# Performance work log

Measured on AMD Instinct MI355X. Metric: run time of the kernel, lower is better.

Reference implementation:

```python
import jax, jax.numpy as jnp
import numpy as np

V, E, H, T, S = 100000, 256, 512, 48, 2048
HD = H // 2  # per-direction hidden size


def _lstm_dir(x, h0, c0, Wih, Whh, b, reverse):
    # Single-direction LSTM over (S, E) input; PyTorch gate order i,f,g,o.
    def step(carry, xt):
        h, c = carry
        z = xt @ Wih.T + h @ Whh.T + b  # (4*HD,)
        i, f, g, o = jnp.split(z, 4)
        i = jax.nn.sigmoid(i)
        f = jax.nn.sigmoid(f)
        g = jnp.tanh(g)
        o = jax.nn.sigmoid(o)
        c = f * c + i * g
        h = o * jnp.tanh(c)
        return (h, c), h
    _, hs = jax.lax.scan(step, (h0, c0), x, reverse=reverse)
    return hs  # (S, HD)


def setup_inputs() -> dict:
    key = jax.random.key(0)
    ks = jax.random.split(key, 12)
    scale = 1.0 / np.sqrt(HD)
    inp = {
        "sent": jax.random.randint(ks[0], (S,), 0, V),
        "embed_table": jax.random.normal(ks[1], (V, E), jnp.float32),
        "Wih_f": jax.random.normal(ks[2], (4 * HD, E), jnp.float32) * scale,
        "Whh_f": jax.random.normal(ks[3], (4 * HD, HD), jnp.float32) * scale,
        "b_f": jax.random.normal(ks[4], (4 * HD,), jnp.float32) * scale,
        "Wih_b": jax.random.normal(ks[5], (4 * HD, E), jnp.float32) * scale,
        "Whh_b": jax.random.normal(ks[6], (4 * HD, HD), jnp.float32) * scale,
        "b_b": jax.random.normal(ks[7], (4 * HD,), jnp.float32) * scale,
        "W_out": jax.random.normal(ks[8], (T, H), jnp.float32) * (1.0 / np.sqrt(H)),
        "b_out": jnp.zeros((T,), jnp.float32),
        "transitions": jax.random.normal(ks[9], (T, T), jnp.float32) * 0.01,
        "h0": jax.random.normal(ks[10], (2, HD), jnp.float32),
        "c0": jax.random.normal(ks[11], (2, HD), jnp.float32),
    }
    return inp


def reference(sent, embed_table, Wih_f, Whh_f, b_f, Wih_b, Whh_b, b_b,
              W_out, b_out, transitions, h0, c0):
    x = embed_table[sent]  # (S, E)
    hf = _lstm_dir(x, h0[0], c0[0], Wih_f, Whh_f, b_f, False)
    hb = _lstm_dir(x, h0[1], c0[1], Wih_b, Whh_b, b_b, True)
    lstm_out = jnp.concatenate([hf, hb], axis=-1)  # (S, H)
    feats = lstm_out @ W_out.T + b_out  # (S, T) emission scores

    # Viterbi forward pass: scores[i,j] = prev[i] + trans[i,j] + obs[j]
    def vstep(prev, obs):
        scores = prev[:, None] + transitions + obs[None, :]
        return jnp.max(scores, axis=0), jnp.argmax(scores, axis=0)
    prev, bps = jax.lax.scan(vstep, feats[0], feats[1:])  # bps: (S-1, T)

    last = jnp.argmax(prev)

    # Backtrack: reverse scan collects the tag at each timestep in order.
    def back(cur, bp):
        p = bp[cur]
        return p, p
    _, prevs = jax.lax.scan(back, last, bps, reverse=True)  # (S-1,)
    path = jnp.concatenate([prevs, last[None]])  # (S,)
    return path
```

## Files before the change

kernel.cpp:

```cpp
#include <hip/hip_runtime.h>
#include <hip/hip_bf16.h>
#include <math.h>

#define S   2048
#define E   256
#define HD  256
#define NCOL 2048
#define NT  48
#define NWG 16

#define XZ_OFF      ((size_t)0)
#define XZ_BYTES    ((size_t)S * 2048 * 4)
#define LSTM_OFF    (XZ_OFF + XZ_BYTES)
#define LSTM_BYTES  ((size_t)S * 512 * 4)
#define FEATS_OFF   (LSTM_OFF + LSTM_BYTES)
#define FEATS_BYTES ((size_t)S * NT * 4)
#define HCUR2_OFF   (FEATS_OFF + FEATS_BYTES)
#define HCUR2_BYTES ((size_t)2 * 2 * 256 * 8)
#define BPS_OFF     (HCUR2_OFF + HCUR2_BYTES)
#define BPS_BYTES   ((size_t)S * NT)
#define PATHA_OFF   (BPS_OFF + BPS_BYTES)
#define PATHA_BYTES ((size_t)3072 * 32)

__device__ __forceinline__ void st_pair_dev(uint2* p, uint2 v) {
    asm volatile("global_store_dwordx2 %0, %1, off sc0 sc1"
                 :: "v"(p), "v"(v) : "memory");
}

__device__ __forceinline__ bool try_h16(const uint2* p, unsigned want,
                                        float h16[16]) {
    uint4 a, b, c, d, e, f, g, h;
    asm volatile(
        "global_load_dwordx4 %0, %8, off sc0 sc1\n\t"
        "global_load_dwordx4 %1, %8, off offset:16 sc0 sc1\n\t"
        "global_load_dwordx4 %2, %8, off offset:32 sc0 sc1\n\t"
        "global_load_dwordx4 %3, %8, off offset:48 sc0 sc1\n\t"
        "global_load_dwordx4 %4, %8, off offset:64 sc0 sc1\n\t"
        "global_load_dwordx4 %5, %8, off offset:80 sc0 sc1\n\t"
        "global_load_dwordx4 %6, %8, off offset:96 sc0 sc1\n\t"
        "global_load_dwordx4 %7, %8, off offset:112 sc0 sc1\n\t"
        "s_waitcnt vmcnt(0)"
        : "=&v"(a), "=&v"(b), "=&v"(c), "=&v"(d),
          "=&v"(e), "=&v"(f), "=&v"(g), "=&v"(h)
        : "v"(p)
        : "memory");
    const unsigned bad =
        (a.y ^ want) | (a.w ^ want) | (b.y ^ want) | (b.w ^ want) |
        (c.y ^ want) | (c.w ^ want) | (d.y ^ want) | (d.w ^ want) |
        (e.y ^ want) | (e.w ^ want) | (f.y ^ want) | (f.w ^ want) |
        (g.y ^ want) | (g.w ^ want) | (h.y ^ want) | (h.w ^ want);
    if (bad) return false;
    h16[0]  = __uint_as_float(a.x); h16[1]  = __uint_as_float(a.z);
    h16[2]  = __uint_as_float(b.x); h16[3]  = __uint_as_float(b.z);
    h16[4]  = __uint_as_float(c.x); h16[5]  = __uint_as_float(c.z);
    h16[6]  = __uint_as_float(d.x); h16[7]  = __uint_as_float(d.z);
    h16[8]  = __uint_as_float(e.x); h16[9]  = __uint_as_float(e.z);
    h16[10] = __uint_as_float(f.x); h16[11] = __uint_as_float(f.z);
    h16[12] = __uint_as_float(g.x); h16[13] = __uint_as_float(g.z);
    h16[14] = __uint_as_float(h.x); h16[15] = __uint_as_float(h.z);
    return true;
}

__global__ __launch_bounds__(256) void gemm_xz(
    const int* __restrict__ sent, const float* __restrict__ emb,
    const float* __restrict__ Wih_f, const float* __restrict__ Wih_b,
    const float* __restrict__ b_f, const float* __restrict__ b_b,
    float* __restrict__ xz)
{
    __shared__ float As[16][132];
    __shared__ float Bs[16][132];
    const int tid = threadIdx.x;
    const int bm = blockIdx.x * 128;
    const int bn = blockIdx.y * 128;
    const int tx = tid & 15, ty = tid >> 4;
    const int lm = tid >> 1, kq = (tid & 1) * 8;

    const int srow = sent[bm + lm];
    const float* arow = emb + (size_t)srow * E;
    const int bcol = bn + lm;
    const float* brow = (bcol < 1024) ? (Wih_f + (size_t)bcol * E)
                                      : (Wih_b + (size_t)(bcol - 1024) * E);
    float acc[8][8];
#pragma unroll
    for (int i = 0; i < 8; ++i)
#pragma unroll
        for (int j = 0; j < 8; ++j) acc[i][j] = 0.f;

    for (int k0 = 0; k0 < 256; k0 += 16) {
        float4 a0 = *(const float4*)(arow + k0 + kq);
        float4 a1 = *(const float4*)(arow + k0 + kq + 4);
        float4 c0v = *(const float4*)(brow + k0 + kq);
        float4 c1v = *(const float4*)(brow + k0 + kq + 4);
        __syncthreads();
        As[kq + 0][lm] = a0.x; As[kq + 1][lm] = a0.y; As[kq + 2][lm] = a0.z; As[kq + 3][lm] = a0.w;
        As[kq + 4][lm] = a1.x; As[kq + 5][lm] = a1.y; As[kq + 6][lm] = a1.z; As[kq + 7][lm] = a1.w;
        Bs[kq + 0][lm] = c0v.x; Bs[kq + 1][lm] = c0v.y; Bs[kq + 2][lm] = c0v.z; Bs[kq + 3][lm] = c0v.w;
        Bs[kq + 4][lm] = c1v.x; Bs[kq + 5][lm] = c1v.y; Bs[kq + 6][lm] = c1v.z; Bs[kq + 7][lm] = c1v.w;
        __syncthreads();
#pragma unroll
        for (int k = 0; k < 16; ++k) {
            float av[8], bv[8];
            *(float4*)&av[0] = *(const float4*)&As[k][ty * 8];
            *(float4*)&av[4] = *(const float4*)&As[k][ty * 8 + 4];
            *(float4*)&bv[0] = *(const float4*)&Bs[k][tx * 8];
            *(float4*)&bv[4] = *(const float4*)&Bs[k][tx * 8 + 4];
#pragma unroll
            for (int i = 0; i < 8; ++i)
#pragma unroll
                for (int j = 0; j < 8; ++j) acc[i][j] += av[i] * bv[j];
        }
    }
    float bias[8];
    const int cb = bn + tx * 8;
    const float* bptr = (cb < 1024) ? (b_f + cb) : (b_b + cb - 1024);
    *(float4*)&bias[0] = *(const float4*)bptr;
    *(float4*)&bias[4] = *(const float4*)(bptr + 4);
#pragma unroll
    for (int i = 0; i < 8; ++i) {
        const int trow = bm + ty * 8 + i;
        float4 o0, o1;
        o0.x = acc[i][0] + bias[0]; o0.y = acc[i][1] + bias[1];
        o0.z = acc[i][2] + bias[2]; o0.w = acc[i][3] + bias[3];
        o1.x = acc[i][4] + bias[4]; o1.y = acc[i][5] + bias[5];
        o1.z = acc[i][6] + bias[6]; o1.w = acc[i][7] + bias[7];
        *(float4*)(xz + (size_t)trow * NCOL + cb) = o0;
        *(float4*)(xz + (size_t)trow * NCOL + cb + 4) = o1;
    }
}

__global__ void __launch_bounds__(256, 1) lstm_rec(
    const float* __restrict__ Whh_f, const float* __restrict__ Whh_b,
    const float* __restrict__ h0, const float* __restrict__ c0,
    const float* __restrict__ xz, uint2* __restrict__ hcur2,
    float* __restrict__ lstm_out)
{
    __shared__ float red[4][16][8];
    __shared__ float actb[128];
    const int wg = blockIdx.x;
    const int dir = wg >> 3;
    const int wi = wg & 7;
    const int ub = wi * 32;
    const int tid = threadIdx.x;
    const int kg = tid >> 4;
    const int rg = tid & 15;
    const int k0 = kg * 16;
    const float* Whh = dir ? Whh_b : Whh_f;

    float w[8][16];
#pragma unroll
    for (int q = 0; q < 8; ++q) {
        const int lr = rg * 8 + q;
        const int grow = (lr >> 5) * 256 + ub + (lr & 31);
        const float* wr = Whh + (size_t)grow * 256 + k0;
#pragma unroll
        for (int kk = 0; kk < 16; kk += 4) {
            float4 v = *(const float4*)(wr + kk);
            w[q][kk] = v.x; w[q][kk + 1] = v.y; w[q][kk + 2] = v.z; w[q][kk + 3] = v.w;
        }
    }
#pragma unroll
    for (int q = 0; q < 8; ++q)
#pragma unroll
        for (int kk = 0; kk < 16; ++kk)
            asm volatile("" : "+v"(w[q][kk]));

    float cst = 0.f;
    if (tid < 32) {
        cst = c0[dir * 256 + ub + tid];
        uint2 iv;
        iv.x = __float_as_uint(h0[dir * 256 + ub + tid]);
        iv.y = 0u;
        st_pair_dev(hcur2 + (size_t)dir * 256 + ub + tid, iv);
    }
    const int zcol = dir * 1024 + (tid >> 5) * 256 + ub + (tid & 31);

    for (int step = 0; step < S; ++step) {
        float xzv = 0.f;
        if (tid < 128) {
            const int tz = dir ? (S - 1 - step) : step;
            xzv = xz[(size_t)tz * NCOL + zcol];
        }
        const uint2* hb = hcur2 + ((size_t)(step & 1) * 2 + dir) * 256 + k0;
        float h16[16];
        while (!try_h16(hb, (unsigned)step, h16)) {}

        float acc[8];
#pragma unroll
        for (int q = 0; q < 8; ++q) acc[q] = 0.f;
#pragma unroll
        for (int kk = 0; kk < 16; ++kk)
#pragma unroll
            for (int q = 0; q < 8; ++q) acc[q] += w[q][kk] * h16[kk];
#pragma unroll
        for (int q = 0; q < 8; ++q) {
            acc[q] += __shfl_xor(acc[q], 16);
            acc[q] += __shfl_xor(acc[q], 32);
        }
        if ((kg & 3) == 0) {
            const int wv = kg >> 2;
#pragma unroll
            for (int q = 0; q < 8; ++q) red[wv][rg][q] = acc[q];
        }
        __syncthreads();
        if (tid < 128) {
            const int rg2 = tid >> 3, q2 = tid & 7;
            const float z = ((red[0][rg2][q2] + red[1][rg2][q2]) +
                             (red[2][rg2][q2] + red[3][rg2][q2])) + xzv;
            const int gate = tid >> 5;
            actb[tid] = (gate == 2) ? tanhf(z) : (1.f / (1.f + expf(-z)));
        }
        __syncthreads();
        if (tid < 32) {
            const int u = tid;
            const float ig = actb[u];
            const float fg = actb[32 + u];
            const float gg = actb[64 + u];
            const float og = actb[96 + u];
            cst = fg * cst + ig * gg;
            const float h = og * tanhf(cst);
            const int tz = dir ? (S - 1 - step) : step;
            uint2 pv;
            pv.x = __float_as_uint(h);
            pv.y = (unsigned)(step + 1);
            st_pair_dev(hcur2 + ((size_t)((step + 1) & 1) * 2 + dir) * 256 + ub + u, pv);
            lstm_out[(size_t)tz * 512 + dir * 256 + ub + u] = h;
        }
    }
}

__global__ __launch_bounds__(256) void feats_k(
    const float* __restrict__ lstm, const float* __restrict__ Wout,
    const float* __restrict__ bout, float* __restrict__ feats)
{
    const int gid = blockIdx.x * 256 + threadIdx.x;
    if (gid >= S * NT) return;
    const int t = gid / NT, tag = gid - t * NT;
    const float* hr = lstm + (size_t)t * 512;
    const float* wr = Wout + (size_t)tag * 512;
    float s0 = 0, s1 = 0, s2 = 0, s3 = 0;
#pragma unroll 4
    for (int k = 0; k < 512; k += 4) {
        float4 h4 = *(const float4*)(hr + k);
        float4 w4 = *(const float4*)(wr + k);
        s0 += h4.x * w4.x; s1 += h4.y * w4.y;
        s2 += h4.z * w4.z; s3 += h4.w * w4.w;
    }
    feats[gid] = (s0 + s1) + (s2 + s3) + bout[tag];
}

__global__ void __launch_bounds__(256, 1) viterbi_k(
    const float* __restrict__ feats, const float* __restrict__ trans,
    unsigned char* __restrict__ bps, unsigned char* __restrict__ pathA,
    int* __restrict__ out)
{
    __shared__ float Tsh[NT * NT];
    __shared__ float vb[2][NT];
    __shared__ unsigned char cmap[64][NT];
    __shared__ int SB[65];
    __shared__ int last_s;
    const int tid = threadIdx.x;

    for (int i = tid; i < NT * NT; i += 256) Tsh[i] = trans[i];
    if (tid < NT) vb[0][tid] = feats[tid];
    __syncthreads();

    if (tid < 64) {
        const bool actj = tid < NT;
        const int j = actj ? tid : 0;
        float obs = feats[NT + j];
        int p = 0;
        for (int t = 1; t < S; ++t) {
            const float obs_n = (t < S - 1) ? feats[(size_t)(t + 1) * NT + j] : 0.f;
            float b0 = -1e30f, b1 = -1e30f, b2 = -1e30f, b3 = -1e30f;
            int i0 = 0, i1 = 12, i2 = 24, i3 = 36;
#pragma unroll
            for (int r = 0; r < 12; ++r) {
                const float s0 = (vb[p][r]      + Tsh[r * NT + j])        + obs;
                const float s1 = (vb[p][12 + r] + Tsh[(12 + r) * NT + j]) + obs;
                const float s2 = (vb[p][24 + r] + Tsh[(24 + r) * NT + j]) + obs;
                const float s3 = (vb[p][36 + r] + Tsh[(36 + r) * NT + j]) + obs;
                if (s0 > b0) { b0 = s0; i0 = r; }
                if (s1 > b1) { b1 = s1; i1 = 12 + r; }
                if (s2 > b2) { b2 = s2; i2 = 24 + r; }
                if (s3 > b3) { b3 = s3; i3 = 36 + r; }
            }
            float best = b0; int bi = i0;
            if (b1 > best) { best = b1; bi = i1; }
            if (b2 > best) { best = b2; bi = i2; }
            if (b3 > best) { best = b3; bi = i3; }

            if (actj) {
                vb[p ^ 1][j] = best;
                bps[(size_t)(t - 1) * NT + j] = (unsigned char)bi;
            }
            asm volatile("s_waitcnt lgkmcnt(0)" ::: "memory");
            __builtin_amdgcn_sched_barrier(0);
            obs = obs_n;
            p ^= 1;
        }
        if (tid == 0) {
            float b = -1e30f; int bi = 0;
            for (int q = 0; q < NT; ++q) { if (vb[p][q] > b) { b = vb[p][q]; bi = q; } }
            last_s = bi;
        }
    }
    __syncthreads();

    int cArr[12], sArr[12];
    unsigned char stv[12];
#pragma unroll
    for (int r = 0; r < 12; ++r) {
        const int task = r * 256 + tid;
        cArr[r] = task / NT;
        sArr[r] = task - cArr[r] * NT;
        stv[r] = (unsigned char)sArr[r];
    }
    for (int stp = 31; stp >= 0; --stp) {
#pragma unroll
        for (int r = 0; r < 12; ++r) {
            const int km = cArr[r] * 32 + stp;
            if (km < S - 1) stv[r] = bps[(size_t)km * NT + stv[r]];
            pathA[(size_t)(cArr[r] * NT + sArr[r]) * 32 + stp] = stv[r];
        }
    }
#pragma unroll
    for (int r = 0; r < 12; ++r) cmap[cArr[r]][sArr[r]] = stv[r];
    __syncthreads();
    if (tid == 0) {
        SB[64] = last_s;
        for (int c = 63; c >= 0; --c) SB[c] = cmap[c][SB[c + 1]];
    }
    __syncthreads();
    for (int t = tid; t < S; t += 256) {
        const int c = t >> 5;
        out[t] = (int)pathA[(size_t)(c * NT + SB[c + 1]) * 32 + (t & 31)];
    }
}

extern "C" void kernel_launch(void* const* d_in, const int* in_sizes, int n_in,
                              void* d_out, int out_size, void* d_ws, size_t ws_size,
                              hipStream_t stream) {
    const int*   sent   = (const int*)d_in[0];
    const float* emb    = (const float*)d_in[1];
    const float* Wih_f  = (const float*)d_in[2];
    const float* Whh_f  = (const float*)d_in[3];
    const float* b_f    = (const float*)d_in[4];
    const float* Wih_b  = (const float*)d_in[5];
    const float* Whh_b  = (const float*)d_in[6];
    const float* b_b    = (const float*)d_in[7];
    const float* W_out  = (const float*)d_in[8];
    const float* b_out  = (const float*)d_in[9];
    const float* trans  = (const float*)d_in[10];
    const float* h0     = (const float*)d_in[11];
    const float* c0     = (const float*)d_in[12];
    int* out = (int*)d_out;

    char* ws = (char*)d_ws;
    float* xz       = (float*)(ws + XZ_OFF);
    float* lstm     = (float*)(ws + LSTM_OFF);
    float* feats    = (float*)(ws + FEATS_OFF);
    uint2* hcur2    = (uint2*)(ws + HCUR2_OFF);
    unsigned char* bps   = (unsigned char*)(ws + BPS_OFF);
    unsigned char* pathA = (unsigned char*)(ws + PATHA_OFF);

    hipMemsetAsync(hcur2, 0xFF, HCUR2_BYTES, stream);

    gemm_xz<<<dim3(16, 16), 256, 0, stream>>>(sent, emb, Wih_f, Wih_b, b_f, b_b, xz);

    lstm_rec<<<dim3(NWG), 256, 0, stream>>>(Whh_f, Whh_b, h0, c0, xz, hcur2, lstm);

    feats_k<<<dim3((S * NT + 255) / 256), 256, 0, stream>>>(lstm, W_out, b_out, feats);

    viterbi_k<<<dim3(1), 256, 0, stream>>>(feats, trans, bps, pathA, out);
}
```

Measured before the change: 6.139 ms.

## Keep Viterbi state in registers and broadcast via wave shuffles

The Viterbi forward loop now keeps each lane's transition column in registers and its running score in a register, broadcasting previous scores across the single 64-lane wave with __shfl instead of a double-buffered LDS array. This drops the per-step LDS stores, the explicit lgkmcnt wait and the schedule barrier on the serial critical path, and the final argmax also uses shuffles. Separately, the LSTM recurrence kernel's launch bound is relaxed to allow two workgroups per CU, which may cap registers and spill its large per-thread weight array.

```diff
diff --git a/kernel.cpp b/kernel.cpp
--- a/kernel.cpp
+++ b/kernel.cpp
@@ -128,7 +128,7 @@
     }
 }
 
-__global__ void __launch_bounds__(256, 1) lstm_rec(
+__global__ void __launch_bounds__(256, 2) lstm_rec(
     const float* __restrict__ Whh_f, const float* __restrict__ Whh_b,
     const float* __restrict__ h0, const float* __restrict__ c0,
     const float* __restrict__ xz, uint2* __restrict__ hcur2,
@@ -253,32 +253,33 @@
     unsigned char* __restrict__ bps, unsigned char* __restrict__ pathA,
     int* __restrict__ out)
 {
-    __shared__ float Tsh[NT * NT];
-    __shared__ float vb[2][NT];
     __shared__ unsigned char cmap[64][NT];
     __shared__ int SB[65];
     __shared__ int last_s;
     const int tid = threadIdx.x;
 
-    for (int i = tid; i < NT * NT; i += 256) Tsh[i] = trans[i];
-    if (tid < NT) vb[0][tid] = feats[tid];
-    __syncthreads();
-
     if (tid < 64) {
         const bool actj = tid < NT;
         const int j = actj ? tid : 0;
+        float T[NT];
+#pragma unroll
+        for (int i = 0; i < NT; ++i) T[i] = trans[i * NT + j];
+        float vself = feats[j];
         float obs = feats[NT + j];
-        int p = 0;
         for (int t = 1; t < S; ++t) {
             const float obs_n = (t < S - 1) ? feats[(size_t)(t + 1) * NT + j] : 0.f;
             float b0 = -1e30f, b1 = -1e30f, b2 = -1e30f, b3 = -1e30f;
             int i0 = 0, i1 = 12, i2 = 24, i3 = 36;
 #pragma unroll
             for (int r = 0; r < 12; ++r) {
-                const float s0 = (vb[p][r]      + Tsh[r * NT + j])        + obs;
-                const float s1 = (vb[p][12 + r] + Tsh[(12 + r) * NT + j]) + obs;
-                const float s2 = (vb[p][24 + r] + Tsh[(24 + r) * NT + j]) + obs;
-                const float s3 = (vb[p][36 + r] + Tsh[(36 + r) * NT + j]) + obs;
+                const float v0 = __shfl(vself, r);
+                const float v1 = __shfl(vself, 12 + r);
+                const float v2 = __shfl(vself, 24 + r);
+                const float v3 = __shfl(vself, 36 + r);
+                const float s0 = (v0 + T[r])      + obs;
+                const float s1 = (v1 + T[12 + r]) + obs;
+                const float s2 = (v2 + T[24 + r]) + obs;
+                const float s3 = (v3 + T[36 + r]) + obs;
                 if (s0 > b0) { b0 = s0; i0 = r; }
                 if (s1 > b1) { b1 = s1; i1 = 12 + r; }
                 if (s2 > b2) { b2 = s2; i2 = 24 + r; }
@@ -290,18 +291,19 @@
             if (b3 > best) { best = b3; bi = i3; }
 
             if (actj) {
-                vb[p ^ 1][j] = best;
                 bps[(size_t)(t - 1) * NT + j] = (unsigned char)bi;
+                vself = best;
             }
-            asm volatile("s_waitcnt lgkmcnt(0)" ::: "memory");
-            __builtin_amdgcn_sched_barrier(0);
             obs = obs_n;
-            p ^= 1;
-        }
-        if (tid == 0) {
-            float b = -1e30f; int bi = 0;
-            for (int q = 0; q < NT; ++q) { if (vb[p][q] > b) { b = vb[p][q]; bi = q; } }
-            last_s = bi;
+        }
+        {
+            float b = __shfl(vself, 0); int bi = 0;
+#pragma unroll
+            for (int q = 1; q < NT; ++q) {
+                const float vq = __shfl(vself, q);
+                if (vq > b) { b = vq; bi = q; }
+            }
+            if (tid == 0) last_s = bi;
         }
     }
     __syncthreads();
```

Result: faster. 5.503 ms (-10.4%).
